# Kernel optimization log

Hardware: AMD Instinct MI355X
Metric: run time of the kernel (lower is better)

Reference implementation:

```python
import jax, jax.numpy as jnp
import numpy as np

B, S, H, E, ID, OD, RD = 128, 256, 512, 128, 30000, 64, 32
IN = H + E + 1 + OD  # rnn_input_dim: weighted + embedded + rate + online feats


def setup_inputs() -> dict:
    key = jax.random.key(0)
    ks = jax.random.split(key, 18)
    sc = 0.02
    inp = {}
    inp['input_id'] = jax.random.randint(ks[0], (B, 1), 0, ID, dtype=jnp.int32)
    inp['input_rate'] = jax.random.uniform(ks[1], (B, 1), jnp.float32)
    inp['hidden'] = jax.random.normal(ks[2], (1, B, H), jnp.float32) * 0.1
    inp['encoder_outputs'] = jax.random.normal(ks[3], (S, B, H), jnp.float32) * 0.1
    inp['attn_mask'] = (jax.random.uniform(ks[4], (B, S)) > 0.3).astype(jnp.int32).at[:, 0].set(1)
    inp['constraint_vec'] = (jax.random.uniform(ks[5], (B, ID)) > 0.5).astype(jnp.float32).at[:, 0].set(1.0)
    inp['online_features'] = jax.random.normal(ks[6], (B, OD), jnp.float32) * 0.1
    inp['rid_features'] = jax.random.normal(ks[7], (B, RD), jnp.float32) * 0.1
    inp['emb'] = jax.random.normal(ks[8], (ID, E), jnp.float32) * sc
    inp['attn_W'] = jax.random.normal(ks[9], (2 * H, H), jnp.float32) * sc
    inp['attn_b'] = jnp.zeros((H,), jnp.float32)
    inp['v_W'] = jax.random.normal(ks[10], (H,), jnp.float32) * sc
    inp['W_ih'] = jax.random.normal(ks[11], (3 * H, IN), jnp.float32) * sc
    inp['b_ih'] = jnp.zeros((3 * H,), jnp.float32)
    inp['W_hh'] = jax.random.normal(ks[12], (3 * H, H), jnp.float32) * sc
    inp['b_hh'] = jnp.zeros((3 * H,), jnp.float32)
    inp['fc_id_W'] = jax.random.normal(ks[13], (ID, H), jnp.float32) * sc
    inp['fc_id_b'] = jnp.zeros((ID,), jnp.float32)
    inp['tan_W'] = jax.random.normal(ks[14], (H, E + H), jnp.float32) * sc
    inp['tan_b'] = jnp.zeros((H,), jnp.float32)
    inp['rate_W'] = jax.random.normal(ks[15], (1, H + RD), jnp.float32) * sc
    inp['rate_b'] = jnp.zeros((1,), jnp.float32)
    return inp


def reference(input_id, input_rate, hidden, encoder_outputs, attn_mask, constraint_vec,
              online_features, rid_features, emb, attn_W, attn_b, v_W, W_ih, b_ih,
              W_hh, b_hh, fc_id_W, fc_id_b, tan_W, tan_b, rate_W, rate_b):
    h = hidden[0]                                    # [B,H]
    embedded = emb[input_id[:, 0]]                   # [B,E] (dropout p=0 -> identity)
    # --- attention ---
    enc = jnp.transpose(encoder_outputs, (1, 0, 2))  # [B,S,H]
    hid_rep = jnp.broadcast_to(h[:, None, :], (B, S, H))
    energy = jnp.tanh(jnp.concatenate([hid_rep, enc], axis=2) @ attn_W + attn_b)  # [B,S,H]
    score = energy @ v_W                             # [B,S]
    score = jnp.where(attn_mask == 0, jnp.float32(-1e10), score)
    a = jax.nn.softmax(score, axis=1)                # [B,S]
    weighted = jnp.einsum('bs,bsh->bh', a, enc)      # [B,H]
    # --- GRU step (torch gate order r,z,n) ---
    rnn_in = jnp.concatenate([weighted, embedded, input_rate, online_features], axis=1)  # [B,IN]
    gi = rnn_in @ W_ih.T + b_ih                      # [B,3H]
    gh = h @ W_hh.T + b_hh                           # [B,3H]
    r = jax.nn.sigmoid(gi[:, :H] + gh[:, :H])
    z = jax.nn.sigmoid(gi[:, H:2 * H] + gh[:, H:2 * H])
    n = jnp.tanh(gi[:, 2 * H:] + r * gh[:, 2 * H:])
    h_new = (1.0 - z) * n + z * h                    # [B,H]
    # --- masked log softmax over id_size ---
    logits = h_new @ fc_id_W.T + fc_id_b             # [B,ID]
    maxes = jnp.max(logits, axis=1, keepdims=True)
    x_exp = jnp.exp(logits - maxes) * constraint_vec
    x_sum = jnp.sum(x_exp, axis=1, keepdims=True)
    ratio_safe = jnp.where(constraint_vec > 0, x_exp / x_sum, 1.0)
    prediction_id = jnp.where(constraint_vec > 0, jnp.log(ratio_safe), -jnp.inf)  # [B,ID]
    # --- tandem rate head ---
    max_id = jnp.argmax(prediction_id, axis=1)
    id_emb = emb[max_id]                             # [B,E]
    rate_in = jax.nn.relu(jnp.concatenate([id_emb, h_new], axis=1) @ tan_W.T + tan_b)  # [B,H]
    prediction_rate = jax.nn.sigmoid(jnp.concatenate([rate_in, rid_features], axis=1) @ rate_W.T + rate_b)  # [B,1]
    return prediction_id, prediction_rate, h_new[None]  # hidden: [1,B,H]
```

## Files before the change

### kernel.cpp

```cpp
#include <hip/hip_runtime.h>
#include <math.h>

typedef __attribute__((ext_vector_type(8))) short short8;
typedef __attribute__((ext_vector_type(4))) float f32x4;
typedef __attribute__((ext_vector_type(4))) unsigned int u32x4;

constexpr int kB  = 128;
constexpr int kS  = 256;
constexpr int kH  = 512;
constexpr int kE  = 128;
constexpr int kID = 30000;
constexpr int kOD = 64;
constexpr int kRD = 32;
constexpr int kIN = kH + kE + 1 + kOD;
constexpr int kG  = 3 * kH;
constexpr int kNC = 10;

constexpr int O_PRE  = 0;
constexpr int O_RNN  = O_PRE + kB * kH;
constexpr int O_GI   = O_RNN + kB * kIN;
constexpr int O_GH   = O_GI + kB * kG;
constexpr int O_HNEW = O_GH + kB * kG;
constexpr int O_W2F  = O_HNEW + kB * kH;
constexpr int O_AH   = O_W2F + 32 * 4096;
constexpr int O_AL   = O_AH + 8 * 4096;
constexpr int O_SM   = O_AL + 8 * 4096;
constexpr int O_SS   = O_SM + kB * kNC;
constexpr int O_SBV  = O_SS + kB * kNC;
constexpr int O_SBI  = O_SBV + kB * kNC;
constexpr int O_ENCF = O_SBI + kB * kNC;
constexpr int O_SC8  = O_GI;
constexpr int O_GP   = O_ENCF;
constexpr int O_GPH  = O_GP + 8 * kB * kG;
constexpr int O_RP   = O_PRE;

constexpr float kNegSentinel = -1.0e30f;

__device__ __forceinline__ float fast_tanh(float x) {
    float e = __expf(2.f * x);
    return 1.f - 2.f / (e + 1.f);
}
__device__ __forceinline__ unsigned int f2bf(float x) {
    unsigned int u = __builtin_bit_cast(unsigned int, x);
    return (u + 0x7fffu + ((u >> 16) & 1u)) >> 16;
}
__device__ __forceinline__ float bfval(float x) {
    return __builtin_bit_cast(float, f2bf(x) << 16);
}
__device__ __forceinline__ unsigned int pack2(float a, float b) {
    return f2bf(a) | (f2bf(b) << 16);
}

__global__ __launch_bounds__(256) void k_prep(
    const float* __restrict__ enc, const float* __restrict__ attn_W,
    const float* __restrict__ attn_b, const float* __restrict__ hidden,
    float* __restrict__ ws, unsigned int* __restrict__ wsu) {
    __shared__ unsigned int SMEM[16 * 260];
    const int blk = blockIdx.x;
    const int tid = threadIdx.x;
    if (blk < 2048) {
        const int l16 = tid & 15;
        const int cb0 = ((tid >> 4) & 3) * 8 + (tid >> 6) * 32;
        const float* rowp = enc + ((size_t)blk * 16 + l16) * kH + cb0;
        unsigned int* dst = wsu + O_ENCF + (size_t)blk * 4096;
        float4 va[4], vb[4];
#pragma unroll
        for (int pass = 0; pass < 4; ++pass) {
            va[pass] = *(const float4*)(rowp + pass * 128);
            vb[pass] = *(const float4*)(rowp + pass * 128 + 4);
        }
#pragma unroll
        for (int pass = 0; pass < 4; ++pass) {
            u32x4 o = {pack2(va[pass].x, va[pass].y), pack2(va[pass].z, va[pass].w),
                       pack2(vb[pass].x, vb[pass].y), pack2(vb[pass].z, vb[pass].w)};
            *(u32x4*)(dst + (pass * 256 + tid) * 4) = o;
        }
    } else if (blk < 2080) {
        const int rbh = blk - 2048;
        const int h0 = rbh * 16;
        const int hh = tid & 15, pg = tid >> 4;
#pragma unroll
        for (int pass = 0; pass < 16; ++pass) {
            int p = pg + pass * 16;
            float a = attn_W[(kH + 2 * p) * kH + h0 + hh];
            float b = attn_W[(kH + 2 * p + 1) * kH + h0 + hh];
            SMEM[hh * 260 + p] = pack2(a, b);
        }
        __syncthreads();
        unsigned int* dst = wsu + O_W2F + (size_t)rbh * 4096;
#pragma unroll
        for (int pass = 0; pass < 4; ++pass) {
            int idx4 = pass * 256 + tid;
            int l16 = idx4 & 15, quad = (idx4 >> 4) & 3, step = idx4 >> 6;
            const unsigned int* p = &SMEM[l16 * 260 + step * 16 + quad * 4];
            u32x4 v = {p[0], p[1], p[2], p[3]};
            *(u32x4*)(dst + idx4 * 4) = v;
        }
    } else {
        float* hl = (float*)SMEM;
        int idx = blk - 2080;
        int b = idx >> 1, half = idx & 1;
        int h = half * 256 + tid;
        hl[tid]       = hidden[b * kH + tid];
        hl[tid + 256] = hidden[b * kH + tid + 256];
        __syncthreads();
        float acc0 = attn_b[h], acc1 = 0.f;
        for (int k0 = 0; k0 < kH; k0 += 16) {
            float wv[16];
#pragma unroll
            for (int j = 0; j < 16; ++j) wv[j] = attn_W[(k0 + j) * kH + h];
#pragma unroll
            for (int j = 0; j < 8; ++j) {
                acc0 += hl[k0 + j] * wv[j];
                acc1 += hl[k0 + 8 + j] * wv[8 + j];
            }
        }
        ws[O_PRE + b * kH + h] = acc0 + acc1;
    }
}

__global__ __launch_bounds__(256) void k_attn(
    const unsigned int* __restrict__ encf, const unsigned int* __restrict__ w2f,
    const float* __restrict__ vW, float* __restrict__ ws) {
    __shared__ float red[128 * 33];
    const int i = blockIdx.x;
    const int s    = (i & 7) + 8 * (i >> 6);
    const int hblk = (i >> 3) & 7;
    const int tid = threadIdx.x;
    const int w = tid >> 6, L = tid & 63;
    const int quad = L >> 4, l16 = L & 15;
    const int wm = w >> 1, wn = w & 1;
    const unsigned int* ap[4];
    const unsigned int* bp[2];
#pragma unroll
    for (int mt = 0; mt < 4; ++mt)
        ap[mt] = encf + (size_t)(s * 8 + wm * 4 + mt) * 4096 + L * 4;
#pragma unroll
    for (int nt = 0; nt < 2; ++nt)
        bp[nt] = w2f + (size_t)(hblk * 4 + wn * 2 + nt) * 4096 + L * 4;
    f32x4 acc[4][2] = {};
    u32x4 abuf[2][4], bbuf[2][2];
#pragma unroll
    for (int t = 0; t < 4; ++t) abuf[0][t] = *(const u32x4*)(ap[t]);
#pragma unroll
    for (int t = 0; t < 2; ++t) bbuf[0][t] = *(const u32x4*)(bp[t]);
#pragma unroll
    for (int step = 0; step < 16; ++step) {
        const int cur = step & 1, nxt = cur ^ 1;
        if (step < 15) {
            const int off = (step + 1) * 256;
#pragma unroll
            for (int t = 0; t < 4; ++t) abuf[nxt][t] = *(const u32x4*)(ap[t] + off);
#pragma unroll
            for (int t = 0; t < 2; ++t) bbuf[nxt][t] = *(const u32x4*)(bp[t] + off);
        }
#pragma unroll
        for (int mt = 0; mt < 4; ++mt)
#pragma unroll
            for (int nt = 0; nt < 2; ++nt)
                acc[mt][nt] = __builtin_amdgcn_mfma_f32_16x16x32_bf16(
                    __builtin_bit_cast(short8, abuf[cur][mt]),
                    __builtin_bit_cast(short8, bbuf[cur][nt]), acc[mt][nt], 0, 0, 0);
    }
#pragma unroll
    for (int mt = 0; mt < 4; ++mt)
#pragma unroll
        for (int rg = 0; rg < 4; ++rg) {
            int row = wm * 64 + mt * 16 + quad * 4 + rg;
            const float* prep = &ws[O_PRE + row * kH + hblk * 64 + wn * 32];
            const float* vp = &vW[hblk * 64 + wn * 32];
            float p = 0.f;
#pragma unroll
            for (int nt = 0; nt < 2; ++nt) {
                int hc = nt * 16 + l16;
                p += vp[hc] * fast_tanh(acc[mt][nt][rg] + prep[hc]);
            }
            red[row * 33 + wn * 16 + l16] = p;
        }
    __syncthreads();
    if (tid < 128) {
        float sum = 0.f;
#pragma unroll
        for (int c = 0; c < 32; ++c) sum += red[tid * 33 + c];
        ws[O_SC8 + hblk * (kB * kS) + tid * kS + s] = sum;
    }
}

__global__ __launch_bounds__(256) void k_soft_weight(
    const float* __restrict__ enc, const int* __restrict__ mask,
    const int* __restrict__ input_id, const float* __restrict__ input_rate,
    const float* __restrict__ online, const float* __restrict__ emb,
    float* __restrict__ ws) {
    int b = blockIdx.x, hg = blockIdx.y, tid = threadIdx.x;
    __shared__ float aa[kS];
    __shared__ float sm[256];
    __shared__ float4 red4[16 * 16];
    float v = 0.f;
#pragma unroll
    for (int h8 = 0; h8 < 8; ++h8)
        v += ws[O_SC8 + h8 * (kB * kS) + b * kS + tid];
    if (mask[b * kS + tid] == 0) v = -1e10f;
    sm[tid] = v;
    __syncthreads();
    for (int o = 128; o > 0; o >>= 1) {
        if (tid < o) sm[tid] = fmaxf(sm[tid], sm[tid + o]);
        __syncthreads();
    }
    float M = sm[0];
    __syncthreads();
    float e = __expf(v - M);
    sm[tid] = e;
    __syncthreads();
    for (int o = 128; o > 0; o >>= 1) {
        if (tid < o) sm[tid] += sm[tid + o];
        __syncthreads();
    }
    aa[tid] = e / sm[0];
    __syncthreads();
    int lane = tid & 15, sg = tid >> 4;
    int col4 = hg * 16 + lane;
    const float4* enc4 = (const float4*)enc;
    float4 acc = {0.f, 0.f, 0.f, 0.f};
    for (int s = sg; s < kS; s += 16) {
        float a = aa[s];
        float4 e4 = enc4[(s * kB + b) * (kH / 4) + col4];
        acc.x += a * e4.x; acc.y += a * e4.y; acc.z += a * e4.z; acc.w += a * e4.w;
    }
    red4[sg * 16 + lane] = acc;
    __syncthreads();
    if (sg == 0) {
        float4 o = {0.f, 0.f, 0.f, 0.f};
#pragma unroll
        for (int j = 0; j < 16; ++j) {
            float4 r = red4[j * 16 + lane];
            o.x += r.x; o.y += r.y; o.z += r.z; o.w += r.w;
        }
        float* dst = &ws[O_RNN + b * kIN + col4 * 4];
        dst[0] = o.x; dst[1] = o.y; dst[2] = o.z; dst[3] = o.w;
    }
    if (hg == 0)
        for (int idx = tid; idx < kE + 1 + kOD; idx += 256) {
            int pos = kH + idx;
            float vv;
            if (idx < kE)       vv = emb[input_id[b] * kE + idx];
            else if (idx == kE) vv = input_rate[b];
            else                vv = online[b * kOD + (idx - kE - 1)];
            ws[O_RNN + b * kIN + pos] = vv;
        }
}

__global__ __launch_bounds__(256, 2) void k_gates(
    const float* __restrict__ rnn, const float* __restrict__ W_ih,
    const float* __restrict__ hid, const float* __restrict__ W_hh,
    float* __restrict__ ws) {
    __shared__ float As[16][132];
    __shared__ float Bs[16][132];
    const float* A;  const float* Bm;  float* Cp;
    int K, kChunk;
    if (blockIdx.y == 0) { A = rnn; Bm = W_ih; Cp = ws + O_GP;  K = kIN; kChunk = 96; }
    else                 { A = hid; Bm = W_hh; Cp = ws + O_GPH; K = kH;  kChunk = 64; }
    Cp += (size_t)blockIdx.z * (kB * kG);
    const int n0 = blockIdx.x * 128;
    const int k0 = blockIdx.z * kChunk;
    const int k1 = min(K, k0 + kChunk);
    const int tid = threadIdx.x;
    const int ri = tid >> 4, ci = tid & 15;
    const int sr = tid >> 1, sc = tid & 1;
    const int nrow = n0 + sr;
    float acc[8][8] = {};
    for (int kt = k0; kt < k1; kt += 16) {
        int kbase = kt + sc * 8;
        if (kt + 16 <= k1) {
            const float* ap = &A[sr * K + kbase];
            float4 a0 = *(const float4*)ap;
            float4 a1 = *(const float4*)(ap + 4);
            As[sc * 8 + 0][sr] = a0.x; As[sc * 8 + 1][sr] = a0.y;
            As[sc * 8 + 2][sr] = a0.z; As[sc * 8 + 3][sr] = a0.w;
            As[sc * 8 + 4][sr] = a1.x; As[sc * 8 + 5][sr] = a1.y;
            As[sc * 8 + 6][sr] = a1.z; As[sc * 8 + 7][sr] = a1.w;
            const float* bp = &Bm[(long)nrow * K + kbase];
            float4 b0 = *(const float4*)bp;
            float4 b1 = *(const float4*)(bp + 4);
            Bs[sc * 8 + 0][sr] = b0.x; Bs[sc * 8 + 1][sr] = b0.y;
            Bs[sc * 8 + 2][sr] = b0.z; Bs[sc * 8 + 3][sr] = b0.w;
            Bs[sc * 8 + 4][sr] = b1.x; Bs[sc * 8 + 5][sr] = b1.y;
            Bs[sc * 8 + 6][sr] = b1.z; Bs[sc * 8 + 7][sr] = b1.w;
        } else {
#pragma unroll
            for (int jj = 0; jj < 8; ++jj) {
                int k = kbase + jj;
                As[sc * 8 + jj][sr] = (k < k1) ? A[sr * K + k] : 0.f;
                Bs[sc * 8 + jj][sr] = (k < k1) ? Bm[(long)nrow * K + k] : 0.f;
            }
        }
        __syncthreads();
#pragma unroll
        for (int kk = 0; kk < 16; ++kk) {
            float a[8], b[8];
            *(float4*)&a[0] = *(const float4*)&As[kk][ri * 4];
            *(float4*)&a[4] = *(const float4*)&As[kk][64 + ri * 4];
            *(float4*)&b[0] = *(const float4*)&Bs[kk][ci * 4];
            *(float4*)&b[4] = *(const float4*)&Bs[kk][64 + ci * 4];
#pragma unroll
            for (int rr = 0; rr < 8; ++rr)
#pragma unroll
                for (int cc = 0; cc < 8; ++cc) acc[rr][cc] += a[rr] * b[cc];
        }
        __syncthreads();
    }
#pragma unroll
    for (int rh = 0; rh < 2; ++rh)
#pragma unroll
        for (int ii = 0; ii < 4; ++ii) {
            int m = rh * 64 + ri * 4 + ii;
#pragma unroll
            for (int ch = 0; ch < 2; ++ch) {
                float4 v = {acc[rh * 4 + ii][ch * 4 + 0], acc[rh * 4 + ii][ch * 4 + 1],
                            acc[rh * 4 + ii][ch * 4 + 2], acc[rh * 4 + ii][ch * 4 + 3]};
                *(float4*)&Cp[(size_t)m * kG + n0 + ch * 64 + ci * 4] = v;
            }
        }
}

__global__ __launch_bounds__(256) void k_gru(const float* __restrict__ hidden,
                                             const float* __restrict__ b_ih,
                                             const float* __restrict__ b_hh,
                                             float* __restrict__ ws,
                                             unsigned int* __restrict__ wsu,
                                             float* __restrict__ outh) {
    int idx = blockIdx.x * 256 + threadIdx.x;
    int b = idx >> 8, pair = idx & 255;
    int j0 = pair * 2;
    const float* gpi = &ws[O_GP  + (size_t)b * kG + j0];
    const float* gph = &ws[O_GPH + (size_t)b * kG + j0];
    float2 gir = {0.f, 0.f}, giz = {0.f, 0.f}, gin = {0.f, 0.f};
    float2 ghr = {0.f, 0.f}, ghz = {0.f, 0.f}, ghn = {0.f, 0.f};
#pragma unroll
    for (int z = 0; z < 8; ++z) {
        size_t off = (size_t)z * (kB * kG);
        float2 a0 = *(const float2*)(gpi + off);
        float2 a1 = *(const float2*)(gpi + off + kH);
        float2 a2 = *(const float2*)(gpi + off + 2 * kH);
        float2 c0 = *(const float2*)(gph + off);
        float2 c1 = *(const float2*)(gph + off + kH);
        float2 c2 = *(const float2*)(gph + off + 2 * kH);
        gir.x += a0.x; gir.y += a0.y; giz.x += a1.x; giz.y += a1.y;
        gin.x += a2.x; gin.y += a2.y;
        ghr.x += c0.x; ghr.y += c0.y; ghz.x += c1.x; ghz.y += c1.y;
        ghn.x += c2.x; ghn.y += c2.y;
    }
    float hn2[2];
#pragma unroll
    for (int t = 0; t < 2; ++t) {
        int j = j0 + t;
        float gi_r = t ? gir.y : gir.x;
        float gi_z = t ? giz.y : giz.x;
        float gi_n = t ? gin.y : gin.x;
        float gh_r = t ? ghr.y : ghr.x;
        float gh_z = t ? ghz.y : ghz.x;
        float gh_n = t ? ghn.y : ghn.x;
        float gr = gi_r + b_ih[j] + gh_r + b_hh[j];
        float gz = gi_z + b_ih[kH + j] + gh_z + b_hh[kH + j];
        float r = 1.f / (1.f + expf(-gr));
        float z = 1.f / (1.f + expf(-gz));
        float n = tanhf(gi_n + b_ih[2 * kH + j] + r * (gh_n + b_hh[2 * kH + j]));
        float hn = (1.f - z) * n + z * hidden[b * kH + j];
        ws[O_HNEW + b * kH + j] = hn;
        outh[b * kH + j] = hn;
        hn2[t] = hn;
    }
    int fidx = (b >> 4) * 4096 +
               ((pair >> 4) * 4 + ((pair >> 2) & 3)) * 64 + (b & 15) * 4 + (pair & 3);
    wsu[O_AH + fidx] = pack2(hn2[0], hn2[1]);
    wsu[O_AL + fidx] = pack2(hn2[0] - bfval(hn2[0]), hn2[1] - bfval(hn2[1]));
}

__global__ __launch_bounds__(256) void k_logits(
    const unsigned int* __restrict__ wsu, const float* __restrict__ Wm,
    const float* __restrict__ bias, float* __restrict__ C) {
    __shared__ unsigned int BH[3][64 * 18];
    __shared__ unsigned int BL[3][64 * 18];
    const unsigned int* Ahp = wsu + O_AH;
    const unsigned int* Alp = wsu + O_AL;
    const int n0 = blockIdx.x * 64;
    const int tid = threadIdx.x;
    const int w = tid >> 6, L = tid & 63;
    const int quad = L >> 4, l16 = L & 15;
    const int r = tid >> 2, seg = tid & 3;
    const int nrow = n0 + r;
    auto stage = [&](int buf, int step) {
        float bv[8] = {};
        if (nrow < kID) {
            const float* bp = &Wm[(long)nrow * kH + step * 32 + seg * 8];
            *(float4*)&bv[0] = *(const float4*)(bp);
            *(float4*)&bv[4] = *(const float4*)(bp + 4);
        }
        unsigned int* dh = &BH[buf][r * 18 + seg * 4];
        unsigned int* dl = &BL[buf][r * 18 + seg * 4];
#pragma unroll
        for (int t = 0; t < 2; ++t) {
            float x0 = bv[4 * t], x1 = bv[4 * t + 1], x2 = bv[4 * t + 2], x3 = bv[4 * t + 3];
            dh[2 * t]     = pack2(x0, x1);
            dh[2 * t + 1] = pack2(x2, x3);
            dl[2 * t]     = pack2(x0 - bfval(x0), x1 - bfval(x1));
            dl[2 * t + 1] = pack2(x2 - bfval(x2), x3 - bfval(x3));
        }
    };
    stage(0, 0);
    stage(1, 1);
    __syncthreads();
    f32x4 acc[2][4] = {};
    for (int step = 0; step < 16; ++step) {
        const int cur = step % 3;
        short8 ah[2], al[2], bh[4], bl[4];
#pragma unroll
        for (int mt = 0; mt < 2; ++mt) {
            int off = (w * 2 + mt) * 4096 + step * 256 + L * 4;
            ah[mt] = __builtin_bit_cast(short8, *(const u32x4*)(Ahp + off));
            al[mt] = __builtin_bit_cast(short8, *(const u32x4*)(Alp + off));
        }
        const unsigned int* ch = BH[cur];
        const unsigned int* cl = BL[cur];
#pragma unroll
        for (int nt = 0; nt < 4; ++nt) {
            const unsigned int* p = ch + (nt * 16 + l16) * 18 + quad * 4;
            uint2 x = *(const uint2*)p, y = *(const uint2*)(p + 2);
            u32x4 u = {x.x, x.y, y.x, y.y};
            bh[nt] = __builtin_bit_cast(short8, u);
            p = cl + (nt * 16 + l16) * 18 + quad * 4;
            x = *(const uint2*)p; y = *(const uint2*)(p + 2);
            u32x4 u2 = {x.x, x.y, y.x, y.y};
            bl[nt] = __builtin_bit_cast(short8, u2);
        }
#pragma unroll
        for (int mt = 0; mt < 2; ++mt)
#pragma unroll
            for (int nt = 0; nt < 4; ++nt) {
                acc[mt][nt] = __builtin_amdgcn_mfma_f32_16x16x32_bf16(
                    al[mt], bh[nt], acc[mt][nt], 0, 0, 0);
                acc[mt][nt] = __builtin_amdgcn_mfma_f32_16x16x32_bf16(
                    ah[mt], bl[nt], acc[mt][nt], 0, 0, 0);
                acc[mt][nt] = __builtin_amdgcn_mfma_f32_16x16x32_bf16(
                    ah[mt], bh[nt], acc[mt][nt], 0, 0, 0);
            }
        if (step + 2 < 16) stage((step + 2) % 3, step + 2);
        __syncthreads();
    }
#pragma unroll
    for (int mt = 0; mt < 2; ++mt)
#pragma unroll
        for (int rg = 0; rg < 4; ++rg) {
            int m = w * 32 + mt * 16 + quad * 4 + rg;
#pragma unroll
            for (int nt = 0; nt < 4; ++nt) {
                int n = n0 + nt * 16 + l16;
                if (n < kID) C[(long)m * kID + n] = acc[mt][nt][rg] + bias[n];
            }
        }
}

__global__ __launch_bounds__(256) void k_stats1(const float* __restrict__ logits,
                                                const float* __restrict__ cvec,
                                                float* __restrict__ ws) {
    int c = blockIdx.x, b = blockIdx.y, tid = threadIdx.x;
    constexpr int chunkE = kID / kNC;
    constexpr int chunk4 = chunkE / 4;
    const float4* lp = (const float4*)(logits + (long)b * kID + c * chunkE);
    const float4* cp = (const float4*)(cvec + (long)b * kID + c * chunkE);
    __shared__ float smm[256], sms[256], smb[256];
    __shared__ int smi[256];
    float m = -INFINITY, s = 0.f, bv = -INFINITY;
    int bi = kID;
    for (int i = tid; i < chunk4; i += 256) {
        float4 l4 = lp[i];
        float4 c4 = cp[i];
        float le[4] = {l4.x, l4.y, l4.z, l4.w};
        float ce[4] = {c4.x, c4.y, c4.z, c4.w};
#pragma unroll
        for (int jj = 0; jj < 4; ++jj) {
            float l = le[jj];
            if (l > m) { s *= __expf(m - l); m = l; }
            if (ce[jj] > 0.f) {
                s += __expf(l - m);
                if (l > bv) { bv = l; bi = c * chunkE + i * 4 + jj; }
            }
        }
    }
    smm[tid] = m; sms[tid] = s; smb[tid] = bv; smi[tid] = bi;
    __syncthreads();
    for (int o = 128; o > 0; o >>= 1) {
        if (tid < o) {
            float m1 = smm[tid], s1 = sms[tid];
            float m2 = smm[tid + o], s2 = sms[tid + o];
            float M = fmaxf(m1, m2);
            sms[tid] = s1 * __expf(m1 - M) + s2 * __expf(m2 - M);
            smm[tid] = M;
            float ov = smb[tid + o]; int oi = smi[tid + o];
            if (ov > smb[tid] || (ov == smb[tid] && oi < smi[tid])) {
                smb[tid] = ov; smi[tid] = oi;
            }
        }
        __syncthreads();
    }
    if (tid == 0) {
        ws[O_SM + b * kNC + c]  = smm[0];
        ws[O_SS + b * kNC + c]  = sms[0];
        ws[O_SBV + b * kNC + c] = smb[0];
        ((int*)ws)[O_SBI + b * kNC + c] = smi[0];
    }
}

__global__ __launch_bounds__(256) void k_finalize(const float* __restrict__ cvec,
                                                  const float* __restrict__ ws,
                                                  float* __restrict__ out) {
    int b = blockIdx.y;
    int i4 = blockIdx.x * 256 + threadIdx.x;
    if (i4 >= kID / 4) return;
    float M = -INFINITY;
#pragma unroll
    for (int c = 0; c < kNC; ++c) M = fmaxf(M, ws[O_SM + b * kNC + c]);
    float S = 0.f;
#pragma unroll
    for (int c = 0; c < kNC; ++c)
        S += ws[O_SS + b * kNC + c] * __expf(ws[O_SM + b * kNC + c] - M);
    float off = M + logf(S);
    float4* op = (float4*)(out + (long)b * kID);
    const float4* cp = (const float4*)(cvec + (long)b * kID);
    float4 l = op[i4];
    float4 c = cp[i4];
    l.x = (c.x > 0.f) ? l.x - off : kNegSentinel;
    l.y = (c.y > 0.f) ? l.y - off : kNegSentinel;
    l.z = (c.z > 0.f) ? l.z - off : kNegSentinel;
    l.w = (c.w > 0.f) ? l.w - off : kNegSentinel;
    op[i4] = l;
}

__global__ __launch_bounds__(256) void k_rate1(
    const float* __restrict__ emb, const float* __restrict__ tanW,
    const float* __restrict__ tanb, const float* __restrict__ rateW,
    float* __restrict__ ws) {
    constexpr int KK = kE + kH;
    int b = blockIdx.x, g = blockIdx.y, tid = threadIdx.x;
    __shared__ float xin[KK];
    __shared__ float red[8];
    float bv = -INFINITY;
    int mid = kID;
#pragma unroll
    for (int c = 0; c < kNC; ++c) {
        float ov = ws[O_SBV + b * kNC + c];
        int oi = ((const int*)ws)[O_SBI + b * kNC + c];
        if (ov > bv || (ov == bv && oi < mid)) { bv = ov; mid = oi; }
    }
    for (int idx = tid; idx < KK; idx += 256)
        xin[idx] = (idx < kE) ? emb[(size_t)mid * kE + idx]
                              : ws[O_HNEW + b * kH + (idx - kE)];
    __syncthreads();
    int grp = tid >> 5, lane = tid & 31;
    int jbase = g * 64 + grp * 8;
    const float* wr = &tanW[(size_t)jbase * KK + lane];
    float acc[8] = {};
#pragma unroll
    for (int t = 0; t < KK / 32; ++t) {
        float xv = xin[lane + 32 * t];
#pragma unroll
        for (int r = 0; r < 8; ++r) acc[r] += xv * wr[r * KK + 32 * t];
    }
    float gsum = 0.f;
#pragma unroll
    for (int r = 0; r < 8; ++r) {
        float a = acc[r];
#pragma unroll
        for (int o = 16; o > 0; o >>= 1) a += __shfl_down(a, o, 32);
        if (lane == 0) gsum += fmaxf(a + tanb[jbase + r], 0.f) * rateW[jbase + r];
    }
    if (lane == 0) red[grp] = gsum;
    __syncthreads();
    if (tid == 0) {
        float s = 0.f;
#pragma unroll
        for (int r = 0; r < 8; ++r) s += red[r];
        ws[O_RP + b * 8 + g] = s;
    }
}

__global__ __launch_bounds__(128) void k_rate2(
    const float* __restrict__ rid, const float* __restrict__ rateW,
    const float* __restrict__ rateb, const float* __restrict__ ws,
    float* __restrict__ out) {
    int b = threadIdx.x;
    float acc = rateb[0];
#pragma unroll
    for (int g = 0; g < 8; ++g) acc += ws[O_RP + b * 8 + g];
#pragma unroll
    for (int k = 0; k < kRD; ++k) acc += rid[b * kRD + k] * rateW[kH + k];
    out[b] = 1.f / (1.f + expf(-acc));
}

extern "C" void kernel_launch(void* const* d_in, const int* in_sizes, int n_in,
                              void* d_out, int out_size, void* d_ws, size_t ws_size,
                              hipStream_t stream) {
    const int*   input_id   = (const int*)  d_in[0];
    const float* input_rate = (const float*)d_in[1];
    const float* hidden     = (const float*)d_in[2];
    const float* enc        = (const float*)d_in[3];
    const int*   attn_mask  = (const int*)  d_in[4];
    const float* cvec       = (const float*)d_in[5];
    const float* online     = (const float*)d_in[6];
    const float* rid        = (const float*)d_in[7];
    const float* emb        = (const float*)d_in[8];
    const float* attn_W     = (const float*)d_in[9];
    const float* attn_b     = (const float*)d_in[10];
    const float* vW         = (const float*)d_in[11];
    const float* W_ih       = (const float*)d_in[12];
    const float* b_ih       = (const float*)d_in[13];
    const float* W_hh       = (const float*)d_in[14];
    const float* b_hh       = (const float*)d_in[15];
    const float* fc_id_W    = (const float*)d_in[16];
    const float* fc_id_b    = (const float*)d_in[17];
    const float* tan_W      = (const float*)d_in[18];
    const float* tan_b      = (const float*)d_in[19];
    const float* rate_W     = (const float*)d_in[20];
    const float* rate_b     = (const float*)d_in[21];

    float* ws         = (float*)d_ws;
    unsigned int* wsu = (unsigned int*)d_ws;
    float* out        = (float*)d_out;
    float* out_pid    = out;
    float* out_rate   = out + kB * kID;
    float* out_h      = out + kB * kID + kB;

    k_prep<<<2336, 256, 0, stream>>>(enc, attn_W, attn_b, hidden, ws, wsu);
    k_attn<<<2048, 256, 0, stream>>>(wsu + O_ENCF, wsu + O_W2F, vW, ws);
    k_soft_weight<<<dim3(128, 8), 256, 0, stream>>>(enc, attn_mask, input_id,
                                                    input_rate, online, emb, ws);
    k_gates<<<dim3(kG / 128, 2, 8), 256, 0, stream>>>(ws + O_RNN, W_ih, hidden, W_hh, ws);
    k_gru<<<128, 256, 0, stream>>>(hidden, b_ih, b_hh, ws, wsu, out_h);
    k_logits<<<dim3((kID + 63) / 64), 256, 0, stream>>>(wsu, fc_id_W, fc_id_b, out_pid);
    k_stats1<<<dim3(kNC, 128), 256, 0, stream>>>(out_pid, cvec, ws);
    k_finalize<<<dim3(30, 128), 256, 0, stream>>>(cvec, ws, out_pid);
    k_rate1<<<dim3(128, 8), 256, 0, stream>>>(emb, tan_W, tan_b, rate_W, ws);
    k_rate2<<<1, 128, 0, stream>>>(rid, rate_W, rate_b, ws, out_rate);
}
```

Before: 355.6 us.

## Convert encoder outputs to bf16 inside attention GEMM instead of a separate prepass

The prep kernel no longer converts the whole encoder_outputs tensor to a bf16 fragment layout in the workspace. The attention kernel now reads fp32 encoder rows directly and packs them to bf16 in registers. The retiling changes each block to one sequence position times 128 hidden columns, with the weight fragments staged through double-buffered LDS, and the reduction is done with shuffles. This removes a full write and re-read of the 64MB encoder tensor and halves the score partials, at the cost of fp32 loads inside the GEMM loop and extra LDS syncs.

```diff
diff --git a/kernel.cpp b/kernel.cpp
--- a/kernel.cpp
+++ b/kernel.cpp
@@ -29,7 +29,7 @@
 constexpr int O_SBV  = O_SS + kB * kNC;
 constexpr int O_SBI  = O_SBV + kB * kNC;
 constexpr int O_ENCF = O_SBI + kB * kNC;
-constexpr int O_SC8  = O_GI;
+constexpr int O_SC4  = O_GI;
 constexpr int O_GP   = O_ENCF;
 constexpr int O_GPH  = O_GP + 8 * kB * kG;
 constexpr int O_RP   = O_PRE;
@@ -52,31 +52,14 @@
 }
 
 __global__ __launch_bounds__(256) void k_prep(
-    const float* __restrict__ enc, const float* __restrict__ attn_W,
-    const float* __restrict__ attn_b, const float* __restrict__ hidden,
-    float* __restrict__ ws, unsigned int* __restrict__ wsu) {
+    const float* __restrict__ attn_W, const float* __restrict__ attn_b,
+    const float* __restrict__ hidden, float* __restrict__ ws,
+    unsigned int* __restrict__ wsu) {
     __shared__ unsigned int SMEM[16 * 260];
     const int blk = blockIdx.x;
     const int tid = threadIdx.x;
-    if (blk < 2048) {
-        const int l16 = tid & 15;
-        const int cb0 = ((tid >> 4) & 3) * 8 + (tid >> 6) * 32;
-        const float* rowp = enc + ((size_t)blk * 16 + l16) * kH + cb0;
-        unsigned int* dst = wsu + O_ENCF + (size_t)blk * 4096;
-        float4 va[4], vb[4];
-#pragma unroll
-        for (int pass = 0; pass < 4; ++pass) {
-            va[pass] = *(const float4*)(rowp + pass * 128);
-            vb[pass] = *(const float4*)(rowp + pass * 128 + 4);
-        }
-#pragma unroll
-        for (int pass = 0; pass < 4; ++pass) {
-            u32x4 o = {pack2(va[pass].x, va[pass].y), pack2(va[pass].z, va[pass].w),
-                       pack2(vb[pass].x, vb[pass].y), pack2(vb[pass].z, vb[pass].w)};
-            *(u32x4*)(dst + (pass * 256 + tid) * 4) = o;
-        }
-    } else if (blk < 2080) {
-        const int rbh = blk - 2048;
+    if (blk < 32) {
+        const int rbh = blk;
         const int h0 = rbh * 16;
         const int hh = tid & 15, pg = tid >> 4;
 #pragma unroll
@@ -98,7 +81,7 @@
         }
     } else {
         float* hl = (float*)SMEM;
-        int idx = blk - 2080;
+        int idx = blk - 32;
         int b = idx >> 1, half = idx & 1;
         int h = half * 256 + tid;
         hl[tid]       = hidden[b * kH + tid];
@@ -120,69 +103,88 @@
 }
 
 __global__ __launch_bounds__(256) void k_attn(
-    const unsigned int* __restrict__ encf, const unsigned int* __restrict__ w2f,
+    const float* __restrict__ enc, const unsigned int* __restrict__ w2f,
     const float* __restrict__ vW, float* __restrict__ ws) {
-    __shared__ float red[128 * 33];
-    const int i = blockIdx.x;
-    const int s    = (i & 7) + 8 * (i >> 6);
-    const int hblk = (i >> 3) & 7;
+    __shared__ unsigned int BS[2][4096];
+    const int bid = blockIdx.x;
+    const int c = bid >> 8;
+    const int s = bid & 255;
     const int tid = threadIdx.x;
     const int w = tid >> 6, L = tid & 63;
     const int quad = L >> 4, l16 = L & 15;
-    const int wm = w >> 1, wn = w & 1;
-    const unsigned int* ap[4];
-    const unsigned int* bp[2];
-#pragma unroll
-    for (int mt = 0; mt < 4; ++mt)
-        ap[mt] = encf + (size_t)(s * 8 + wm * 4 + mt) * 4096 + L * 4;
-#pragma unroll
-    for (int nt = 0; nt < 2; ++nt)
-        bp[nt] = w2f + (size_t)(hblk * 4 + wn * 2 + nt) * 4096 + L * 4;
-    f32x4 acc[4][2] = {};
-    u32x4 abuf[2][4], bbuf[2][2];
-#pragma unroll
-    for (int t = 0; t < 4; ++t) abuf[0][t] = *(const u32x4*)(ap[t]);
-#pragma unroll
-    for (int t = 0; t < 2; ++t) bbuf[0][t] = *(const u32x4*)(bp[t]);
-#pragma unroll
-    for (int step = 0; step < 16; ++step) {
-        const int cur = step & 1, nxt = cur ^ 1;
-        if (step < 15) {
-            const int off = (step + 1) * 256;
-#pragma unroll
-            for (int t = 0; t < 4; ++t) abuf[nxt][t] = *(const u32x4*)(ap[t] + off);
-#pragma unroll
-            for (int t = 0; t < 2; ++t) bbuf[nxt][t] = *(const u32x4*)(bp[t] + off);
-        }
-#pragma unroll
-        for (int mt = 0; mt < 4; ++mt)
-#pragma unroll
-            for (int nt = 0; nt < 2; ++nt)
-                acc[mt][nt] = __builtin_amdgcn_mfma_f32_16x16x32_bf16(
-                    __builtin_bit_cast(short8, abuf[cur][mt]),
-                    __builtin_bit_cast(short8, bbuf[cur][nt]), acc[mt][nt], 0, 0, 0);
-    }
-#pragma unroll
-    for (int mt = 0; mt < 4; ++mt)
+    const float* arow[2];
+#pragma unroll
+    for (int mt = 0; mt < 2; ++mt) {
+        int b = (w * 2 + mt) * 16 + l16;
+        arow[mt] = enc + ((size_t)s * kB + b) * kH + quad * 8;
+    }
+    const unsigned int* wbase = w2f + (size_t)(c * 8) * 4096;
+    u32x4 sreg[4];
+    auto ld_group = [&](int g) {
+#pragma unroll
+        for (int k2 = 0; k2 < 4; ++k2) {
+            int i = tid + k2 * 256;
+            int nt = i >> 7, st = (i >> 6) & 1, u = i & 63;
+            sreg[k2] = *(const u32x4*)(wbase + (size_t)nt * 4096 + (g * 2 + st) * 256 + u * 4);
+        }
+    };
+    auto st_group = [&](int buf) {
+#pragma unroll
+        for (int k2 = 0; k2 < 4; ++k2)
+            *(u32x4*)&BS[buf][(tid + k2 * 256) * 4] = sreg[k2];
+    };
+    f32x4 acc[2][8] = {};
+    ld_group(0);
+    st_group(0);
+    __syncthreads();
+    for (int g = 0; g < 8; ++g) {
+        if (g < 7) ld_group(g + 1);
+        const int buf = g & 1;
+#pragma unroll
+        for (int st = 0; st < 2; ++st) {
+            const int step = g * 2 + st;
+            short8 af[2];
+#pragma unroll
+            for (int mt = 0; mt < 2; ++mt) {
+                float4 x = *(const float4*)(arow[mt] + step * 32);
+                float4 y = *(const float4*)(arow[mt] + step * 32 + 4);
+                u32x4 u = {pack2(x.x, x.y), pack2(x.z, x.w),
+                           pack2(y.x, y.y), pack2(y.z, y.w)};
+                af[mt] = __builtin_bit_cast(short8, u);
+            }
+#pragma unroll
+            for (int nt = 0; nt < 8; ++nt) {
+                u32x4 bv = *(const u32x4*)&BS[buf][(nt * 2 + st) * 256 + L * 4];
+                short8 bf = __builtin_bit_cast(short8, bv);
+#pragma unroll
+                for (int mt = 0; mt < 2; ++mt)
+                    acc[mt][nt] = __builtin_amdgcn_mfma_f32_16x16x32_bf16(
+                        af[mt], bf, acc[mt][nt], 0, 0, 0);
+            }
+        }
+        __syncthreads();
+        if (g < 7) st_group((g + 1) & 1);
+        __syncthreads();
+    }
+    const float* vp = vW + c * 128;
+#pragma unroll
+    for (int mt = 0; mt < 2; ++mt) {
+        int tm = w * 2 + mt;
 #pragma unroll
         for (int rg = 0; rg < 4; ++rg) {
-            int row = wm * 64 + mt * 16 + quad * 4 + rg;
-            const float* prep = &ws[O_PRE + row * kH + hblk * 64 + wn * 32];
-            const float* vp = &vW[hblk * 64 + wn * 32];
+            int row = tm * 16 + quad * 4 + rg;
+            const float* prep = &ws[O_PRE + row * kH + c * 128];
             float p = 0.f;
 #pragma unroll
-            for (int nt = 0; nt < 2; ++nt) {
+            for (int nt = 0; nt < 8; ++nt) {
                 int hc = nt * 16 + l16;
                 p += vp[hc] * fast_tanh(acc[mt][nt][rg] + prep[hc]);
             }
-            red[row * 33 + wn * 16 + l16] = p;
-        }
-    __syncthreads();
-    if (tid < 128) {
-        float sum = 0.f;
-#pragma unroll
-        for (int c = 0; c < 32; ++c) sum += red[tid * 33 + c];
-        ws[O_SC8 + hblk * (kB * kS) + tid * kS + s] = sum;
+#pragma unroll
+            for (int o = 1; o < 16; o <<= 1) p += __shfl_xor(p, o, 64);
+            if (l16 == 0)
+                ws[O_SC4 + c * (kB * kS) + row * kS + s] = p;
+        }
     }
 }
 
@@ -197,8 +199,8 @@
     __shared__ float4 red4[16 * 16];
     float v = 0.f;
 #pragma unroll
-    for (int h8 = 0; h8 < 8; ++h8)
-        v += ws[O_SC8 + h8 * (kB * kS) + b * kS + tid];
+    for (int h4 = 0; h4 < 4; ++h4)
+        v += ws[O_SC4 + h4 * (kB * kS) + b * kS + tid];
     if (mask[b * kS + tid] == 0) v = -1e10f;
     sm[tid] = v;
     __syncthreads();
@@ -629,8 +631,8 @@
     float* out_rate   = out + kB * kID;
     float* out_h      = out + kB * kID + kB;
 
-    k_prep<<<2336, 256, 0, stream>>>(enc, attn_W, attn_b, hidden, ws, wsu);
-    k_attn<<<2048, 256, 0, stream>>>(wsu + O_ENCF, wsu + O_W2F, vW, ws);
+    k_prep<<<288, 256, 0, stream>>>(attn_W, attn_b, hidden, ws, wsu);
+    k_attn<<<1024, 256, 0, stream>>>(enc, wsu + O_W2F, vW, ws);
     k_soft_weight<<<dim3(128, 8), 256, 0, stream>>>(enc, attn_mask, input_id,
                                                     input_rate, online, emb, ws);
     k_gates<<<dim3(kG / 128, 2, 8), 256, 0, stream>>>(ws + O_RNN, W_ih, hidden, W_hh, ws);
```

New measurement: 362.8 us. 1.02x slower.

## Fuse encoder bf16 conversion into attention MFMA kernel, drop pre-pass

Applied to the files above, without the earlier changes.

Removes the separate k_prep pass that converted the encoder outputs to a bf16 fragment layout in workspace. k_attn now reads fp32 encoder rows directly and packs them to bf16 in registers with the hardware v_cvt_pk_bf16_f32 instruction before each MFMA. This avoids writing and rereading a 32 MB bf16 copy. In exchange, each attention block loads twice the bytes of fp32 A data, and every hblk block rereads the same encoder rows, eight times in total, so cache reuse matters. It also doubles the register buffer size.

```diff
diff --git a/kernel.cpp b/kernel.cpp
--- a/kernel.cpp
+++ b/kernel.cpp
@@ -50,33 +50,21 @@
 __device__ __forceinline__ unsigned int pack2(float a, float b) {
     return f2bf(a) | (f2bf(b) << 16);
 }
+__device__ __forceinline__ unsigned int pack2hw(float a, float b) {
+    unsigned int r;
+    asm("v_cvt_pk_bf16_f32 %0, %1, %2" : "=v"(r) : "v"(a), "v"(b));
+    return r;
+}
 
 __global__ __launch_bounds__(256) void k_prep(
-    const float* __restrict__ enc, const float* __restrict__ attn_W,
-    const float* __restrict__ attn_b, const float* __restrict__ hidden,
-    float* __restrict__ ws, unsigned int* __restrict__ wsu) {
+    const float* __restrict__ attn_W, const float* __restrict__ attn_b,
+    const float* __restrict__ hidden, float* __restrict__ ws,
+    unsigned int* __restrict__ wsu) {
     __shared__ unsigned int SMEM[16 * 260];
     const int blk = blockIdx.x;
     const int tid = threadIdx.x;
-    if (blk < 2048) {
-        const int l16 = tid & 15;
-        const int cb0 = ((tid >> 4) & 3) * 8 + (tid >> 6) * 32;
-        const float* rowp = enc + ((size_t)blk * 16 + l16) * kH + cb0;
-        unsigned int* dst = wsu + O_ENCF + (size_t)blk * 4096;
-        float4 va[4], vb[4];
-#pragma unroll
-        for (int pass = 0; pass < 4; ++pass) {
-            va[pass] = *(const float4*)(rowp + pass * 128);
-            vb[pass] = *(const float4*)(rowp + pass * 128 + 4);
-        }
-#pragma unroll
-        for (int pass = 0; pass < 4; ++pass) {
-            u32x4 o = {pack2(va[pass].x, va[pass].y), pack2(va[pass].z, va[pass].w),
-                       pack2(vb[pass].x, vb[pass].y), pack2(vb[pass].z, vb[pass].w)};
-            *(u32x4*)(dst + (pass * 256 + tid) * 4) = o;
-        }
-    } else if (blk < 2080) {
-        const int rbh = blk - 2048;
+    if (blk < 32) {
+        const int rbh = blk;
         const int h0 = rbh * 16;
         const int hh = tid & 15, pg = tid >> 4;
 #pragma unroll
@@ -98,7 +86,7 @@
         }
     } else {
         float* hl = (float*)SMEM;
-        int idx = blk - 2080;
+        int idx = blk - 32;
         int b = idx >> 1, half = idx & 1;
         int h = half * 256 + tid;
         hl[tid]       = hidden[b * kH + tid];
@@ -120,7 +108,7 @@
 }
 
 __global__ __launch_bounds__(256) void k_attn(
-    const unsigned int* __restrict__ encf, const unsigned int* __restrict__ w2f,
+    const float* __restrict__ enc, const unsigned int* __restrict__ w2f,
     const float* __restrict__ vW, float* __restrict__ ws) {
     __shared__ float red[128 * 33];
     const int i = blockIdx.x;
@@ -130,37 +118,49 @@
     const int w = tid >> 6, L = tid & 63;
     const int quad = L >> 4, l16 = L & 15;
     const int wm = w >> 1, wn = w & 1;
-    const unsigned int* ap[4];
+    const float* ap[4];
     const unsigned int* bp[2];
 #pragma unroll
     for (int mt = 0; mt < 4; ++mt)
-        ap[mt] = encf + (size_t)(s * 8 + wm * 4 + mt) * 4096 + L * 4;
+        ap[mt] = enc + ((size_t)s * kB + (wm * 4 + mt) * 16 + l16) * kH + quad * 8;
 #pragma unroll
     for (int nt = 0; nt < 2; ++nt)
         bp[nt] = w2f + (size_t)(hblk * 4 + wn * 2 + nt) * 4096 + L * 4;
     f32x4 acc[4][2] = {};
-    u32x4 abuf[2][4], bbuf[2][2];
-#pragma unroll
-    for (int t = 0; t < 4; ++t) abuf[0][t] = *(const u32x4*)(ap[t]);
+    float4 abuf[2][4][2];
+    u32x4 bbuf[2][2];
+#pragma unroll
+    for (int t = 0; t < 4; ++t) {
+        abuf[0][t][0] = *(const float4*)(ap[t]);
+        abuf[0][t][1] = *(const float4*)(ap[t] + 4);
+    }
 #pragma unroll
     for (int t = 0; t < 2; ++t) bbuf[0][t] = *(const u32x4*)(bp[t]);
 #pragma unroll
     for (int step = 0; step < 16; ++step) {
         const int cur = step & 1, nxt = cur ^ 1;
         if (step < 15) {
-            const int off = (step + 1) * 256;
-#pragma unroll
-            for (int t = 0; t < 4; ++t) abuf[nxt][t] = *(const u32x4*)(ap[t] + off);
-#pragma unroll
-            for (int t = 0; t < 2; ++t) bbuf[nxt][t] = *(const u32x4*)(bp[t] + off);
-        }
-#pragma unroll
-        for (int mt = 0; mt < 4; ++mt)
+            const int aoff = (step + 1) * 32;
+            const int boff = (step + 1) * 256;
+#pragma unroll
+            for (int t = 0; t < 4; ++t) {
+                abuf[nxt][t][0] = *(const float4*)(ap[t] + aoff);
+                abuf[nxt][t][1] = *(const float4*)(ap[t] + aoff + 4);
+            }
+#pragma unroll
+            for (int t = 0; t < 2; ++t) bbuf[nxt][t] = *(const u32x4*)(bp[t] + boff);
+        }
+#pragma unroll
+        for (int mt = 0; mt < 4; ++mt) {
+            float4 x = abuf[cur][mt][0], y = abuf[cur][mt][1];
+            u32x4 u = {pack2hw(x.x, x.y), pack2hw(x.z, x.w),
+                       pack2hw(y.x, y.y), pack2hw(y.z, y.w)};
+            short8 af = __builtin_bit_cast(short8, u);
 #pragma unroll
             for (int nt = 0; nt < 2; ++nt)
                 acc[mt][nt] = __builtin_amdgcn_mfma_f32_16x16x32_bf16(
-                    __builtin_bit_cast(short8, abuf[cur][mt]),
-                    __builtin_bit_cast(short8, bbuf[cur][nt]), acc[mt][nt], 0, 0, 0);
+                    af, __builtin_bit_cast(short8, bbuf[cur][nt]), acc[mt][nt], 0, 0, 0);
+        }
     }
 #pragma unroll
     for (int mt = 0; mt < 4; ++mt)
@@ -629,8 +629,8 @@
     float* out_rate   = out + kB * kID;
     float* out_h      = out + kB * kID + kB;
 
-    k_prep<<<2336, 256, 0, stream>>>(enc, attn_W, attn_b, hidden, ws, wsu);
-    k_attn<<<2048, 256, 0, stream>>>(wsu + O_ENCF, wsu + O_W2F, vW, ws);
+    k_prep<<<288, 256, 0, stream>>>(attn_W, attn_b, hidden, ws, wsu);
+    k_attn<<<2048, 256, 0, stream>>>(enc, wsu + O_W2F, vW, ws);
     k_soft_weight<<<dim3(128, 8), 256, 0, stream>>>(enc, attn_mask, input_id,
                                                     input_rate, online, emb, ws);
     k_gates<<<dim3(kG / 128, 2, 8), 256, 0, stream>>>(ws + O_RNN, W_ih, hidden, W_hh, ws);
```

Result: slower. 428.3 us (+20.4%).
